# Performance work log

Hardware: AMD Instinct MI355X
Metric: run time of the kernel (lower is better)

The kernel has to match this reference:

```python
import jax, jax.numpy as jnp
import numpy as np

H, KV, D, WIN = 16, 4, 128, 1024


def _rope(x, cos, sin):
    # x: [B, H, S, D]; cos/sin: [1, 1, S, D//2]
    d = x.shape[-1] // 2
    x1, x2 = x[..., :d], x[..., d:]
    S = x.shape[2]
    c, s = cos[:, :, :S], sin[:, :, :S]
    return jnp.concatenate([x1 * c + x2 * s, -x1 * s + x2 * c], axis=-1)


def _rms_norm(x):
    eps = jnp.finfo(x.dtype).eps
    return x * jax.lax.rsqrt(jnp.mean(jnp.square(x), axis=-1, keepdims=True) + eps)


def setup_inputs() -> dict:
    key = jax.random.key(0)
    ks = jax.random.split(key, 7)
    B, S, E = 2, 2048, 2048
    return {
        "x": jax.random.normal(ks[0], (B, S, E), jnp.float32),
        "cos": jax.random.normal(ks[1], (1, 1, S, D // 2), jnp.float32),
        "sin": jax.random.normal(ks[2], (1, 1, S, D // 2), jnp.float32),
        "Wq": jax.random.normal(ks[3], (H * D, E), jnp.float32) * 0.02,
        "Wk": jax.random.normal(ks[4], (KV * D, E), jnp.float32) * 0.02,
        "Wv": jax.random.normal(ks[5], (KV * D, E), jnp.float32) * 0.02,
        "Wo": jax.random.normal(ks[6], (E, H * D), jnp.float32) * 0.02,
    }


def reference(x, cos, sin, Wq, Wk, Wv, Wo):
    B, S, E = x.shape
    rep = H // KV
    # projections -> [B, heads, S, D]
    q = (x @ Wq.T).reshape(B, S, H, D).transpose(0, 2, 1, 3)
    k = (x @ Wk.T).reshape(B, S, KV, D).transpose(0, 2, 1, 3)
    v = (x @ Wv.T).reshape(B, S, KV, D).transpose(0, 2, 1, 3)
    # GQA: materialize repeated K/V heads (matches repeat_interleave)
    k = jnp.repeat(k, rep, axis=1)
    v = jnp.repeat(v, rep, axis=1)
    # RoPE then QK RMSNorm (no learned scale)
    q = _rms_norm(_rope(q, cos, sin))
    k = _rms_norm(_rope(k, cos, sin))
    scores = jnp.einsum("bhqd,bhkd->bhqk", q, k) * (D ** -0.5)
    # causal & sliding-window mask
    i = jnp.arange(S)[:, None]
    j = jnp.arange(S)[None, :]
    mask = (i >= j) & (jnp.abs(i - j) < WIN)
    scores = jnp.where(mask[None, None], scores, -jnp.inf)
    attn = jax.nn.softmax(scores, axis=-1)
    out = jnp.einsum("bhqk,bhkd->bhqd", attn, v)
    out = out.transpose(0, 2, 1, 3).reshape(B, S, H * D)
    return out @ Wo.T
```

## Files before the change

kernel.cpp:

```cpp
#include <hip/hip_runtime.h>
#include <stdint.h>

using bf16 = __bf16;
typedef __bf16 bf16x8 __attribute__((ext_vector_type(8)));
typedef __bf16 bf16x4 __attribute__((ext_vector_type(4)));
typedef float f32x4 __attribute__((ext_vector_type(4)));

#define H_ 16
#define KV_ 4
#define D_ 128
#define WIN_ 1024
#define B_ 2
#define S_ 2048
#define E_ 2048
#define HD_ 2048
#define NQKV_ 3072

__device__ __forceinline__ void gld_lds16(const void* gptr, void* lptr) {
    __builtin_amdgcn_global_load_lds(
        (__attribute__((address_space(1))) void*)(uintptr_t)gptr,
        (__attribute__((address_space(3))) void*)(uintptr_t)lptr, 16, 0, 0);
}

__global__ __launch_bounds__(256) void cvt_f32_bf16(const float* __restrict__ src,
                                                    bf16* __restrict__ dst, int n) {
    int i = (blockIdx.x * 256 + threadIdx.x) * 4;
    if (i >= n) return;
    const float4 v = *(const float4*)(src + i);
    bf16x4 o = {(bf16)v.x, (bf16)v.y, (bf16)v.z, (bf16)v.w};
    *(bf16x4*)(dst + i) = o;
}

template <typename OutT>
__global__ __launch_bounds__(256) void gemm_bt(const bf16* __restrict__ A,
                                               const bf16* __restrict__ W,
                                               OutT* __restrict__ C, int K, int ldc) {
    __shared__ alignas(16) bf16 As[128 * 32];
    __shared__ alignas(16) bf16 Bs[128 * 32];
    const int t = threadIdx.x;
    const int lane = t & 63;
    const int wave = t >> 6;
    const int l15 = lane & 15;
    const int quad = lane >> 4;
    const int wm = (wave & 1) * 64;
    const int wn = (wave >> 1) * 64;
    const int m0 = blockIdx.x * 128;
    const int n0 = blockIdx.y * 128;

    f32x4 acc[4][4] = {};

    const int sr = t >> 2;
    const int sc = (t & 3) * 8;
    const bf16* Ap = A + (size_t)(m0 + sr) * K + sc;
    const bf16* Wp = W + (size_t)(n0 + sr) * K + sc;
    bf16* As0 = &As[t * 8];
    bf16* As1 = &As[64 * 32 + t * 8];
    bf16* Bs0 = &Bs[t * 8];
    bf16* Bs1 = &Bs[64 * 32 + t * 8];
    const size_t rowskip = (size_t)64 * K;

    for (int k0 = 0; k0 < K; k0 += 32) {
        gld_lds16(Ap + k0, As0);
        gld_lds16(Ap + k0 + rowskip, As1);
        gld_lds16(Wp + k0, Bs0);
        gld_lds16(Wp + k0 + rowskip, Bs1);
        __syncthreads();
        bf16x8 af[4], bfr[4];
#pragma unroll
        for (int i = 0; i < 4; ++i) {
            af[i] = *(const bf16x8*)&As[(wm + i * 16 + l15) * 32 + quad * 8];
            bfr[i] = *(const bf16x8*)&Bs[(wn + i * 16 + l15) * 32 + quad * 8];
        }
#pragma unroll
        for (int i = 0; i < 4; ++i)
#pragma unroll
            for (int j = 0; j < 4; ++j)
                acc[i][j] =
                    __builtin_amdgcn_mfma_f32_16x16x32_bf16(af[i], bfr[j], acc[i][j], 0, 0, 0);
        __syncthreads();
    }
#pragma unroll
    for (int i = 0; i < 4; ++i) {
        const int row = m0 + wm + i * 16 + quad * 4;
#pragma unroll
        for (int j = 0; j < 4; ++j) {
            const int col = n0 + wn + j * 16 + l15;
#pragma unroll
            for (int r = 0; r < 4; ++r) C[(size_t)(row + r) * ldc + col] = (OutT)acc[i][j][r];
        }
    }
}

__global__ __launch_bounds__(256) void rope_norm(const bf16* __restrict__ qkv,
                                                 const float* __restrict__ cosp,
                                                 const float* __restrict__ sinp,
                                                 bf16* __restrict__ qn, bf16* __restrict__ kn,
                                                 bf16* __restrict__ vt) {
    const int unit = blockIdx.x * 4 + (threadIdx.x >> 6);
    const int lane = threadIdx.x & 63;
    const int b = unit / (S_ * 24);
    const int rem = unit - b * (S_ * 24);
    const int s = rem / 24;
    const int j = rem - s * 24;
    const size_t rowbase = (size_t)(b * S_ + s) * NQKV_;
    const float eps = 1.1920929e-7f;

    if (j < 20) {
        const bf16* src = qkv + rowbase + ((j < 16) ? (j * 128) : (2048 + (j - 16) * 128));
        float x1 = (float)src[lane];
        float x2 = (float)src[lane + 64];
        float c = cosp[s * 64 + lane];
        float sn = sinp[s * 64 + lane];
        float y1 = x1 * c + x2 * sn;
        float y2 = -x1 * sn + x2 * c;
        float ss = y1 * y1 + y2 * y2;
#pragma unroll
        for (int off = 1; off < 64; off <<= 1) ss += __shfl_xor(ss, off, 64);
        float r = rsqrtf(ss * (1.0f / 128.0f) + eps);
        if (j < 16) {
            r *= 0.12751740f;
            bf16* dst = qn + (size_t)((b * H_ + j) * S_ + s) * 128;
            dst[lane] = (bf16)(y1 * r);
            dst[lane + 64] = (bf16)(y2 * r);
        } else {
            bf16* dst = kn + (size_t)((b * KV_ + (j - 16)) * S_ + s) * 128;
            dst[lane] = (bf16)(y1 * r);
            dst[lane + 64] = (bf16)(y2 * r);
        }
    } else {
        const int jv = j - 20;
        const bf16* src = qkv + rowbase + 2560 + jv * 128;
        bf16* dst = vt + (size_t)(b * KV_ + jv) * 128 * S_ + s;
        dst[(size_t)lane * S_] = src[lane];
        dst[(size_t)(lane + 64) * S_] = src[lane + 64];
    }
}

__global__ __launch_bounds__(256, 4) void attn_fwd(const bf16* __restrict__ Qn,
                                                   const bf16* __restrict__ Kn,
                                                   const bf16* __restrict__ Vt,
                                                   bf16* __restrict__ Out) {
    __shared__ alignas(16) bf16 Ks[64 * 128];
    __shared__ alignas(16) bf16 Vs[128 * 64];
    __shared__ alignas(16) bf16 Ps[4 * 16 * 64];

    const int t = threadIdx.x;
    const int lane = t & 63;
    const int wave = t >> 6;
    const int l15 = lane & 15;
    const int quad = lane >> 4;
    const int swz = l15 & 7;
    const int qb0 = blockIdx.x * 64;
    const int h = blockIdx.y;
    const int b = blockIdx.z;
    const int hk = h >> 2;
    const int qw0 = qb0 + wave * 16;

    const bf16* qbase = Qn + ((size_t)((b * H_ + h) * S_) + qw0 + l15) * 128;
    bf16x8 qf[4];
#pragma unroll
    for (int c4 = 0; c4 < 4; ++c4) qf[c4] = *(const bf16x8*)(qbase + c4 * 32 + quad * 8);

    f32x4 o[8] = {};
    float m = -1e30f, lsum = 0.0f;

    const bf16* kroot = Kn + (size_t)((b * KV_ + hk) * S_) * 128;
    const bf16* vroot = Vt + (size_t)((b * KV_ + hk) * 128) * S_;

    const int ku = (t & 15) ^ ((t >> 4) & 7);
    const int krow = t >> 4;
    const int vu = (t & 7) ^ ((t >> 3) & 7);
    const int vrow = t >> 3;
    const bf16* kst = kroot + (size_t)krow * 128 + ku * 8;
    const bf16* vst = vroot + (size_t)vrow * S_ + vu * 8;
    bf16* ksl = &Ks[t * 8];
    bf16* vsl = &Vs[t * 8];

    int lo = qb0 - (WIN_ - 1);
    if (lo < 0) lo = 0;
    const int kb_start = lo & ~63;
    const int kb_end = qb0 + 64;

    for (int kb = kb_start; kb < kb_end; kb += 64) {
#pragma unroll
        for (int c = 0; c < 4; ++c) gld_lds16(kst + (size_t)(kb + c * 16) * 128, ksl + c * 2048);
#pragma unroll
        for (int c = 0; c < 4; ++c) gld_lds16(vst + (size_t)(c * 32) * S_ + kb, vsl + c * 2048);
        __syncthreads();

        const bool wave_active = (kb + 63 >= qw0 - (WIN_ - 1));
        if (wave_active) {
            f32x4 sacc[4] = {};
#pragma unroll
            for (int kblk = 0; kblk < 4; ++kblk)
#pragma unroll
                for (int c4 = 0; c4 < 4; ++c4) {
                    bf16x8 kf = *(const bf16x8*)&Ks[(kblk * 16 + l15) * 128 +
                                                    (((c4 * 4 + quad) ^ swz) * 8)];
                    sacc[kblk] =
                        __builtin_amdgcn_mfma_f32_16x16x32_bf16(kf, qf[c4], sacc[kblk], 0, 0, 0);
                }

            const int q = qw0 + l15;
            float sv[16];
            const bool interior = (kb + 63 <= qw0) && (kb >= qw0 + 15 - (WIN_ - 1));
            if (interior) {
#pragma unroll
                for (int kblk = 0; kblk < 4; ++kblk)
#pragma unroll
                    for (int r = 0; r < 4; ++r) sv[kblk * 4 + r] = sacc[kblk][r];
            } else {
#pragma unroll
                for (int kblk = 0; kblk < 4; ++kblk)
#pragma unroll
                    for (int r = 0; r < 4; ++r) {
                        const int key = kb + kblk * 16 + quad * 4 + r;
                        const bool valid = (key <= q) && (q - key < WIN_);
                        sv[kblk * 4 + r] = valid ? sacc[kblk][r] : -1e30f;
                    }
            }
            float mc = sv[0];
#pragma unroll
            for (int i = 1; i < 16; ++i) mc = fmaxf(mc, sv[i]);
            mc = fmaxf(mc, __shfl_xor(mc, 16, 64));
            mc = fmaxf(mc, __shfl_xor(mc, 32, 64));
            const float mnew = fmaxf(m, mc);
            const float al = __builtin_amdgcn_exp2f(m - mnew);
            float ls = 0.0f;
#pragma unroll
            for (int i = 0; i < 16; ++i) {
                sv[i] = __builtin_amdgcn_exp2f(sv[i] - mnew);
                ls += sv[i];
            }
            ls += __shfl_xor(ls, 16, 64);
            ls += __shfl_xor(ls, 32, 64);
            lsum = lsum * al + ls;
            m = mnew;
#pragma unroll
            for (int dblk = 0; dblk < 8; ++dblk) o[dblk] *= al;

            bf16* pw = &Ps[wave * 1024 + l15 * 64];
#pragma unroll
            for (int kblk = 0; kblk < 4; ++kblk) {
                bf16x4 pb = {(bf16)sv[kblk * 4 + 0], (bf16)sv[kblk * 4 + 1],
                             (bf16)sv[kblk * 4 + 2], (bf16)sv[kblk * 4 + 3]};
                const int phys = (kblk * 2 + (quad >> 1)) ^ swz;
                *(bf16x4*)&pw[phys * 8 + (quad & 1) * 4] = pb;
            }
#pragma unroll
            for (int kc = 0; kc < 2; ++kc) {
                const int up = ((kc * 4 + quad) ^ swz) * 8;
                bf16x8 pfv = *(const bf16x8*)&pw[up];
#pragma unroll
                for (int dblk = 0; dblk < 8; ++dblk) {
                    bf16x8 vf = *(const bf16x8*)&Vs[(dblk * 16 + l15) * 64 + up];
                    o[dblk] = __builtin_amdgcn_mfma_f32_16x16x32_bf16(vf, pfv, o[dblk], 0, 0, 0);
                }
            }
        }
        __syncthreads();
    }

    const float inv = 1.0f / lsum;
    const int q = qw0 + l15;
    bf16* ob = Out + (size_t)(b * S_ + q) * HD_ + h * 128;
#pragma unroll
    for (int dblk = 0; dblk < 8; ++dblk) {
        bf16x4 ov = {(bf16)(o[dblk][0] * inv), (bf16)(o[dblk][1] * inv),
                     (bf16)(o[dblk][2] * inv), (bf16)(o[dblk][3] * inv)};
        *(bf16x4*)&ob[dblk * 16 + quad * 4] = ov;
    }
}

extern "C" void kernel_launch(void* const* d_in, const int* in_sizes, int n_in, void* d_out,
                              int out_size, void* d_ws, size_t ws_size, hipStream_t stream) {
    const float* x = (const float*)d_in[0];
    const float* cosp = (const float*)d_in[1];
    const float* sinp = (const float*)d_in[2];
    const float* Wq = (const float*)d_in[3];
    const float* Wk = (const float*)d_in[4];
    const float* Wv = (const float*)d_in[5];
    const float* Wo = (const float*)d_in[6];
    float* out = (float*)d_out;

    constexpr size_t MB = 1ull << 20;
    char* ws = (char*)d_ws;
    bf16* xb    = (bf16*)(ws + 0);
    bf16* wqkv  = (bf16*)(ws + 16 * MB);
    bf16* wo    = (bf16*)(ws + 28 * MB);
    bf16* qkv   = (bf16*)(ws + 36 * MB);
    bf16* qn    = (bf16*)(ws + 60 * MB);
    bf16* kn    = (bf16*)(ws + 76 * MB);
    bf16* vt    = (bf16*)(ws + 80 * MB);
    bf16* attnb = (bf16*)(ws + 84 * MB);

    cvt_f32_bf16<<<8192, 256, 0, stream>>>(x, xb, 8388608);
    cvt_f32_bf16<<<4096, 256, 0, stream>>>(Wq, wqkv, 4194304);
    cvt_f32_bf16<<<1024, 256, 0, stream>>>(Wk, wqkv + 4194304, 1048576);
    cvt_f32_bf16<<<1024, 256, 0, stream>>>(Wv, wqkv + 5242880, 1048576);
    cvt_f32_bf16<<<4096, 256, 0, stream>>>(Wo, wo, 4194304);

    gemm_bt<bf16><<<dim3(32, 24), 256, 0, stream>>>(xb, wqkv, qkv, 2048, 3072);
    rope_norm<<<24576, 256, 0, stream>>>(qkv, cosp, sinp, qn, kn, vt);
    attn_fwd<<<dim3(32, 16, 2), 256, 0, stream>>>(qn, kn, vt, attnb);
    gemm_bt<float><<<dim3(32, 16), 256, 0, stream>>>(attnb, wo, out, 2048, 2048);
}
```

Measured before the change: 330.7 us.

## Fuse RoPE/RMSNorm/V-transpose into QKV GEMM epilogue, merge casts, swizzle LDS

Replaces the separate rope_norm kernel with an epilogue in the QKV GEMM that stages the tile in LDS and applies RoPE, RMSNorm, scaling and the V transpose before writing out. This removes the intermediate qkv buffer round trip and the scattered per-element transposed stores. The five f32-to-bf16 conversion launches are merged into one kernel. The GEMM LDS reads are XOR-swizzled to reduce bank conflicts. The extra 34KB LDS staging buffer may reduce occupancy of the QKV GEMM.

```diff
diff --git a/kernel.cpp b/kernel.cpp
--- a/kernel.cpp
+++ b/kernel.cpp
@@ -14,7 +14,6 @@
 #define S_ 2048
 #define E_ 2048
 #define HD_ 2048
-#define NQKV_ 3072
 
 __device__ __forceinline__ void gld_lds16(const void* gptr, void* lptr) {
     __builtin_amdgcn_global_load_lds(
@@ -22,14 +21,25 @@
         (__attribute__((address_space(3))) void*)(uintptr_t)lptr, 16, 0, 0);
 }
 
-__global__ __launch_bounds__(256) void cvt_f32_bf16(const float* __restrict__ src,
-                                                    bf16* __restrict__ dst, int n) {
+__global__ __launch_bounds__(256) void cvt_all(const float* __restrict__ x,
+                                               const float* __restrict__ wq,
+                                               const float* __restrict__ wk,
+                                               const float* __restrict__ wv,
+                                               const float* __restrict__ wo,
+                                               bf16* __restrict__ dst) {
     int i = (blockIdx.x * 256 + threadIdx.x) * 4;
-    if (i >= n) return;
-    const float4 v = *(const float4*)(src + i);
+    const float* src;
+    int off;
+    if (i < 8388608)       { src = x;  off = 0; }
+    else if (i < 12582912) { src = wq; off = 8388608; }
+    else if (i < 13631488) { src = wk; off = 12582912; }
+    else if (i < 14680064) { src = wv; off = 13631488; }
+    else                   { src = wo; off = 14680064; }
+    const float4 v = *(const float4*)(src + (i - off));
     bf16x4 o = {(bf16)v.x, (bf16)v.y, (bf16)v.z, (bf16)v.w};
     *(bf16x4*)(dst + i) = o;
 }
+
 
 template <typename OutT>
 __global__ __launch_bounds__(256) void gemm_bt(const bf16* __restrict__ A,
@@ -42,6 +52,7 @@
     const int wave = t >> 6;
     const int l15 = lane & 15;
     const int quad = lane >> 4;
+    const int fsw = (l15 >> 1) & 3;
     const int wm = (wave & 1) * 64;
     const int wn = (wave >> 1) * 64;
     const int m0 = blockIdx.x * 128;
@@ -50,7 +61,7 @@
     f32x4 acc[4][4] = {};
 
     const int sr = t >> 2;
-    const int sc = (t & 3) * 8;
+    const int sc = ((t & 3) ^ ((t >> 3) & 3)) * 8;
     const bf16* Ap = A + (size_t)(m0 + sr) * K + sc;
     const bf16* Wp = W + (size_t)(n0 + sr) * K + sc;
     bf16* As0 = &As[t * 8];
@@ -68,8 +79,8 @@
         bf16x8 af[4], bfr[4];
 #pragma unroll
         for (int i = 0; i < 4; ++i) {
-            af[i] = *(const bf16x8*)&As[(wm + i * 16 + l15) * 32 + quad * 8];
-            bfr[i] = *(const bf16x8*)&Bs[(wn + i * 16 + l15) * 32 + quad * 8];
+            af[i] = *(const bf16x8*)&As[(wm + i * 16 + l15) * 32 + ((quad ^ fsw) * 8)];
+            bfr[i] = *(const bf16x8*)&Bs[(wn + i * 16 + l15) * 32 + ((quad ^ fsw) * 8)];
         }
 #pragma unroll
         for (int i = 0; i < 4; ++i)
@@ -91,48 +102,137 @@
     }
 }
 
-__global__ __launch_bounds__(256) void rope_norm(const bf16* __restrict__ qkv,
-                                                 const float* __restrict__ cosp,
-                                                 const float* __restrict__ sinp,
-                                                 bf16* __restrict__ qn, bf16* __restrict__ kn,
-                                                 bf16* __restrict__ vt) {
-    const int unit = blockIdx.x * 4 + (threadIdx.x >> 6);
-    const int lane = threadIdx.x & 63;
-    const int b = unit / (S_ * 24);
-    const int rem = unit - b * (S_ * 24);
-    const int s = rem / 24;
-    const int j = rem - s * 24;
-    const size_t rowbase = (size_t)(b * S_ + s) * NQKV_;
-    const float eps = 1.1920929e-7f;
-
-    if (j < 20) {
-        const bf16* src = qkv + rowbase + ((j < 16) ? (j * 128) : (2048 + (j - 16) * 128));
-        float x1 = (float)src[lane];
-        float x2 = (float)src[lane + 64];
-        float c = cosp[s * 64 + lane];
-        float sn = sinp[s * 64 + lane];
-        float y1 = x1 * c + x2 * sn;
-        float y2 = -x1 * sn + x2 * c;
-        float ss = y1 * y1 + y2 * y2;
-#pragma unroll
-        for (int off = 1; off < 64; off <<= 1) ss += __shfl_xor(ss, off, 64);
-        float r = rsqrtf(ss * (1.0f / 128.0f) + eps);
-        if (j < 16) {
-            r *= 0.12751740f;
-            bf16* dst = qn + (size_t)((b * H_ + j) * S_ + s) * 128;
-            dst[lane] = (bf16)(y1 * r);
-            dst[lane + 64] = (bf16)(y2 * r);
+__global__ __launch_bounds__(256) void gemm_qkv_rope(const bf16* __restrict__ A,
+                                                     const bf16* __restrict__ W,
+                                                     const float* __restrict__ cosp,
+                                                     const float* __restrict__ sinp,
+                                                     bf16* __restrict__ qn,
+                                                     bf16* __restrict__ kn,
+                                                     bf16* __restrict__ vt) {
+    __shared__ alignas(16) bf16 As[128 * 32];
+    __shared__ alignas(16) bf16 Bs[128 * 32];
+    __shared__ alignas(16) bf16 Cs[128 * 136];
+    const int t = threadIdx.x;
+    const int lane = t & 63;
+    const int wave = t >> 6;
+    const int l15 = lane & 15;
+    const int quad = lane >> 4;
+    const int fsw = (l15 >> 1) & 3;
+    const int wm = (wave & 1) * 64;
+    const int wn = (wave >> 1) * 64;
+    const int m0 = blockIdx.x * 128;
+    const int n0 = blockIdx.y * 128;
+    const int K = E_;
+
+    f32x4 acc[4][4] = {};
+
+    const int sr = t >> 2;
+    const int sc = ((t & 3) ^ ((t >> 3) & 3)) * 8;
+    const bf16* Ap = A + (size_t)(m0 + sr) * K + sc;
+    const bf16* Wp = W + (size_t)(n0 + sr) * K + sc;
+    bf16* As0 = &As[t * 8];
+    bf16* As1 = &As[64 * 32 + t * 8];
+    bf16* Bs0 = &Bs[t * 8];
+    bf16* Bs1 = &Bs[64 * 32 + t * 8];
+    const size_t rowskip = (size_t)64 * K;
+
+    for (int k0 = 0; k0 < K; k0 += 32) {
+        gld_lds16(Ap + k0, As0);
+        gld_lds16(Ap + k0 + rowskip, As1);
+        gld_lds16(Wp + k0, Bs0);
+        gld_lds16(Wp + k0 + rowskip, Bs1);
+        __syncthreads();
+        bf16x8 af[4], bfr[4];
+#pragma unroll
+        for (int i = 0; i < 4; ++i) {
+            af[i] = *(const bf16x8*)&As[(wm + i * 16 + l15) * 32 + ((quad ^ fsw) * 8)];
+            bfr[i] = *(const bf16x8*)&Bs[(wn + i * 16 + l15) * 32 + ((quad ^ fsw) * 8)];
+        }
+#pragma unroll
+        for (int i = 0; i < 4; ++i)
+#pragma unroll
+            for (int j = 0; j < 4; ++j)
+                acc[i][j] =
+                    __builtin_amdgcn_mfma_f32_16x16x32_bf16(af[i], bfr[j], acc[i][j], 0, 0, 0);
+        __syncthreads();
+    }
+
+#pragma unroll
+    for (int i = 0; i < 4; ++i) {
+        const int row = wm + i * 16 + quad * 4;
+#pragma unroll
+        for (int j = 0; j < 4; ++j) {
+            const int col = wn + j * 16 + l15;
+#pragma unroll
+            for (int r = 0; r < 4; ++r) Cs[(row + r) * 136 + col] = (bf16)acc[i][j][r];
+        }
+    }
+    __syncthreads();
+
+    const int unit = n0 >> 7;
+    if (unit < 20) {
+        const int row = t >> 1;
+        const int half = t & 1;
+        const int gr = m0 + row;
+        const int bb = gr >> 11;
+        const int s = gr & 2047;
+        const bf16* crow = &Cs[row * 136 + half * 32];
+        const float* cp = cosp + s * 64 + half * 32;
+        const float* sp = sinp + s * 64 + half * 32;
+        bf16x8 xa[4], xb2[4];
+#pragma unroll
+        for (int u = 0; u < 4; ++u) {
+            xa[u] = *(const bf16x8*)(crow + u * 8);
+            xb2[u] = *(const bf16x8*)(crow + 64 + u * 8);
+        }
+        float y1[32], y2[32], ss = 0.0f;
+#pragma unroll
+        for (int u = 0; u < 4; ++u)
+#pragma unroll
+            for (int e = 0; e < 8; ++e) {
+                const int jj = u * 8 + e;
+                const float x1 = (float)xa[u][e];
+                const float x2 = (float)xb2[u][e];
+                const float c = cp[jj];
+                const float sn = sp[jj];
+                y1[jj] = x1 * c + x2 * sn;
+                y2[jj] = x2 * c - x1 * sn;
+                ss += y1[jj] * y1[jj] + y2[jj] * y2[jj];
+            }
+        ss += __shfl_xor(ss, 1, 64);
+        float rr = rsqrtf(ss * (1.0f / 128.0f) + 1.1920929e-7f);
+        bf16* dst;
+        if (unit < 16) {
+            rr *= 0.12751740f;
+            dst = qn + ((size_t)(bb * H_ + unit) * S_ + s) * 128 + half * 32;
         } else {
-            bf16* dst = kn + (size_t)((b * KV_ + (j - 16)) * S_ + s) * 128;
-            dst[lane] = (bf16)(y1 * r);
-            dst[lane + 64] = (bf16)(y2 * r);
+            dst = kn + ((size_t)(bb * KV_ + (unit - 16)) * S_ + s) * 128 + half * 32;
+        }
+#pragma unroll
+        for (int u = 0; u < 4; ++u) {
+            bf16x8 p1, p2;
+#pragma unroll
+            for (int e = 0; e < 8; ++e) {
+                p1[e] = (bf16)(y1[u * 8 + e] * rr);
+                p2[e] = (bf16)(y2[u * 8 + e] * rr);
+            }
+            *(bf16x8*)(dst + u * 8) = p1;
+            *(bf16x8*)(dst + 64 + u * 8) = p2;
         }
     } else {
-        const int jv = j - 20;
-        const bf16* src = qkv + rowbase + 2560 + jv * 128;
-        bf16* dst = vt + (size_t)(b * KV_ + jv) * 128 * S_ + s;
-        dst[(size_t)lane * S_] = src[lane];
-        dst[(size_t)(lane + 64) * S_] = src[lane + 64];
+        const int jv = unit - 20;
+        const int d = t >> 1;
+        const int sl0 = (t & 1) * 64;
+        const int s0 = (m0 & 2047) + sl0;
+        const int bb = m0 >> 11;
+        bf16* vdst = vt + ((size_t)(bb * KV_ + jv) * 128 + d) * S_ + s0;
+#pragma unroll
+        for (int u = 0; u < 8; ++u) {
+            bf16x8 pk;
+#pragma unroll
+            for (int e = 0; e < 8; ++e) pk[e] = Cs[(sl0 + u * 8 + e) * 136 + d];
+            *(bf16x8*)(vdst + u * 8) = pk;
+        }
     }
 }
 
@@ -288,20 +388,13 @@
     bf16* xb    = (bf16*)(ws + 0);
     bf16* wqkv  = (bf16*)(ws + 16 * MB);
     bf16* wo    = (bf16*)(ws + 28 * MB);
-    bf16* qkv   = (bf16*)(ws + 36 * MB);
-    bf16* qn    = (bf16*)(ws + 60 * MB);
-    bf16* kn    = (bf16*)(ws + 76 * MB);
-    bf16* vt    = (bf16*)(ws + 80 * MB);
-    bf16* attnb = (bf16*)(ws + 84 * MB);
-
-    cvt_f32_bf16<<<8192, 256, 0, stream>>>(x, xb, 8388608);
-    cvt_f32_bf16<<<4096, 256, 0, stream>>>(Wq, wqkv, 4194304);
-    cvt_f32_bf16<<<1024, 256, 0, stream>>>(Wk, wqkv + 4194304, 1048576);
-    cvt_f32_bf16<<<1024, 256, 0, stream>>>(Wv, wqkv + 5242880, 1048576);
-    cvt_f32_bf16<<<4096, 256, 0, stream>>>(Wo, wo, 4194304);
-
-    gemm_bt<bf16><<<dim3(32, 24), 256, 0, stream>>>(xb, wqkv, qkv, 2048, 3072);
-    rope_norm<<<24576, 256, 0, stream>>>(qkv, cosp, sinp, qn, kn, vt);
+    bf16* qn    = (bf16*)(ws + 40 * MB);
+    bf16* kn    = (bf16*)(ws + 56 * MB);
+    bf16* vt    = (bf16*)(ws + 60 * MB);
+    bf16* attnb = (bf16*)(ws + 64 * MB);
+
+    cvt_all<<<18432, 256, 0, stream>>>(x, Wq, Wk, Wv, Wo, xb);
+    gemm_qkv_rope<<<dim3(32, 24), 256, 0, stream>>>(xb, wqkv, cosp, sinp, qn, kn, vt);
     attn_fwd<<<dim3(32, 16, 2), 256, 0, stream>>>(qn, kn, vt, attnb);
     gemm_bt<float><<<dim3(32, 16), 256, 0, stream>>>(attnb, wo, out, 2048, 2048);
 }
```

Result: faster. 311.8 us (-5.7%).
